# Performance work log

Hardware: AMD Instinct MI355X
Metric: run time of the kernel (lower is better)

The kernel has to match this reference:

```python
import jax, jax.numpy as jnp
import numpy as np

# --- config-derived constants (match init_kwargs) ---
BATCH = 16
TEMP = 0.1
N_REGIONS = 9
IMG = 512
NUM_FILTERS = 5      # len(no_filters)-1
N_DEC_BLOCKS = 2
SIZE_FACTOR = 1 << (NUM_FILTERS - N_DEC_BLOCKS)   # 8
IM = IMG // SIZE_FACTOR - 4                        # 60
H = W = IM + 2                                     # 62 (feature map spatial size)
C = 512
EPS = 1e-6

_h = IM // 2  # 30
_X = _Y = IM  # 60
POS = np.array([[0,0],[0,_h],[0,_Y],[_h,0],[_h,_h],[_h,_Y],[_X,0],[_X,_h],[_X,_Y]], np.int32)
NEG = np.array([
  [[0,_h],[_h,0],[_h,_h],[0,_Y],[_X,0]],
  [[0,0],[0,_Y],[_h,0],[_h,_h],[_h,_Y]],
  [[0,0],[0,_h],[_h,_h],[_h,_Y],[_X,_Y]],
  [[0,0],[0,_h],[_h,_h],[_X,0],[_X,_h]],
  [[0,0],[0,_h],[_h,0],[_h,_Y],[_X,_h]],
  [[0,_h],[0,_Y],[_h,_h],[_X,_h],[_X,_Y]],
  [[0,0],[_h,0],[_h,_h],[_X,_h],[_X,_Y]],
  [[_h,0],[_h,_h],[_h,_Y],[_X,0],[_X,_Y]],
  [[0,_Y],[_h,_h],[_h,_Y],[_X,0],[_X,_h]],
], np.int32)

def _patch_flat(idx):
    # idx [..., 2] (row, col) -> flat indices of the 2x2 patch, [..., 4]
    base = idx[..., 0] * W + idx[..., 1]
    return np.stack([base, base + 1, base + W, base + W + 1], axis=-1)

POS_FLAT = jnp.asarray(_patch_flat(POS))     # [9, 4]
NEG_FLAT = jnp.asarray(_patch_flat(NEG))     # [9, 5, 4]

def _cos(a, b):
    # cosine similarity over last axis, torch-style eps clamp on the norm product
    dot = jnp.sum(a * b, axis=-1)
    na = jnp.sqrt(jnp.sum(a * a, axis=-1))
    nb = jnp.sqrt(jnp.sum(b * b, axis=-1))
    return dot / jnp.maximum(na * nb, EPS)


def setup_inputs() -> dict:
    key = jax.random.key(0)
    x = jax.random.normal(key, (BATCH, C, H, W), dtype=jnp.float32)
    return {"x": x}


def reference(x):
    B = x.shape[0]
    xf = x.reshape(B, C, H * W)
    pp = xf[:, :, POS_FLAT]   # [B, C, 9, 4]
    nn_ = xf[:, :, NEG_FLAT]  # [B, C, 9, 5, 4]
    i1p, i2p = pp[0::2], pp[1::2]      # [P, C, 9, 4]
    i1n, i2n = nn_[0::2], nn_[1::2]    # [P, C, 9, 5, 4]

    # positive similarity (symmetric: cos(i1,i2) == cos(i2,i1))
    num_ss = _cos(i1p, i2p) / TEMP                 # [P, C, 9]
    S = jnp.sum(jnp.exp(num_ss), axis=1)           # [P, 9]

    a1 = i1p[:, :, :, None, :]                     # [P, C, 9, 1, 4]
    a2 = i2p[:, :, :, None, :]
    den1 = jnp.exp(_cos(a1, i1n) / TEMP) + jnp.exp(_cos(a1, i2n) / TEMP)  # [P, C, 9, 5]
    den2 = jnp.exp(_cos(a2, i2n) / TEMP) + jnp.exp(_cos(a2, i1n) / TEMP)
    D1 = jnp.sum(den1, axis=(1, 3))                # [P, 9]
    D2 = jnp.sum(den2, axis=(1, 3))

    loss = jnp.sum(-jnp.log(S / (S + D1)) - jnp.log(S / (S + D2)))
    return loss / B / N_REGIONS
```

## Files before the change

kernel.cpp:

```cpp
#include <hip/hip_runtime.h>
#include <math.h>

#define NPAIR 8
#define NREG 9
#define NCH 512
#define HW 3844
#define W62 62

__constant__ int POS_BASE[9] = {0, 30, 60, 1860, 1890, 1920, 3720, 3750, 3780};
__constant__ int NEG_BASE[9][5] = {
    {30, 1860, 1890, 60, 3720},
    {0, 60, 1860, 1890, 1920},
    {0, 30, 1890, 1920, 3780},
    {0, 30, 1890, 3720, 3750},
    {0, 30, 1860, 1920, 3750},
    {30, 60, 1890, 3750, 3780},
    {0, 1860, 1890, 3750, 3780},
    {1860, 1890, 1920, 3720, 3780},
    {60, 1890, 1920, 3720, 3750}};

__device__ __forceinline__ void load_patch(const float* __restrict__ p, int base, float v[4]) {
    float2 a = *(const float2*)(p + base);
    float2 b = *(const float2*)(p + base + W62);
    v[0] = a.x; v[1] = a.y; v[2] = b.x; v[3] = b.y;
}

__device__ __forceinline__ float dot4(const float* a, const float* b) {
    return a[0] * b[0] + a[1] * b[1] + a[2] * b[2] + a[3] * b[3];
}

__device__ __forceinline__ float wave_sum(float v) {
    #pragma unroll
    for (int off = 32; off > 0; off >>= 1) v += __shfl_down(v, off, 64);
    return v;
}

__global__ __launch_bounds__(512) void lcl_partial(const float* __restrict__ x,
                                                   float* __restrict__ ws) {
    const int blk = blockIdx.x;
    const int p = blk / NREG;
    const int r = blk % NREG;
    const int c = threadIdx.x;

    const float* p1 = x + ((size_t)(2 * p) * NCH + c) * HW;
    const float* p2 = x + ((size_t)(2 * p + 1) * NCH + c) * HW;

    float v1[4], v2[4], n1[5][4], n2[5][4];
    const int pb = POS_BASE[r];
    load_patch(p1, pb, v1);
    load_patch(p2, pb, v2);
    #pragma unroll
    for (int j = 0; j < 5; j++) {
        const int nb = NEG_BASE[r][j];
        load_patch(p1, nb, n1[j]);
        load_patch(p2, nb, n2[j]);
    }

    const float nv1 = dot4(v1, v1);
    const float nv2 = dot4(v2, v2);

    float s = expf(10.0f * dot4(v1, v2) / fmaxf(sqrtf(nv1 * nv2), 1e-6f));
    float d1 = 0.0f, d2 = 0.0f;
    #pragma unroll
    for (int j = 0; j < 5; j++) {
        const float nn1 = dot4(n1[j], n1[j]);
        const float nn2 = dot4(n2[j], n2[j]);
        d1 += expf(10.0f * dot4(v1, n1[j]) / fmaxf(sqrtf(nv1 * nn1), 1e-6f));
        d1 += expf(10.0f * dot4(v1, n2[j]) / fmaxf(sqrtf(nv1 * nn2), 1e-6f));
        d2 += expf(10.0f * dot4(v2, n2[j]) / fmaxf(sqrtf(nv2 * nn2), 1e-6f));
        d2 += expf(10.0f * dot4(v2, n1[j]) / fmaxf(sqrtf(nv2 * nn1), 1e-6f));
    }

    s = wave_sum(s);
    d1 = wave_sum(d1);
    d2 = wave_sum(d2);

    __shared__ float sm[3][8];
    const int wave = threadIdx.x >> 6;
    const int lane = threadIdx.x & 63;
    if (lane == 0) { sm[0][wave] = s; sm[1][wave] = d1; sm[2][wave] = d2; }
    __syncthreads();
    if (threadIdx.x == 0) {
        float S = 0.0f, D1 = 0.0f, D2 = 0.0f;
        #pragma unroll
        for (int w = 0; w < 8; w++) { S += sm[0][w]; D1 += sm[1][w]; D2 += sm[2][w]; }
        ws[blk] = logf(S + D1) + logf(S + D2) - 2.0f * logf(S);
    }
}

__global__ __launch_bounds__(64) void lcl_final(const float* __restrict__ ws,
                                                float* __restrict__ out) {
    const int t = threadIdx.x;
    float v = ws[t];
    if (t + 64 < NPAIR * NREG) v += ws[t + 64];
    v = wave_sum(v);
    if (t == 0) out[0] = v * (1.0f / 144.0f);
}

extern "C" void kernel_launch(void* const* d_in, const int* in_sizes, int n_in,
                              void* d_out, int out_size, void* d_ws, size_t ws_size,
                              hipStream_t stream) {
    const float* x = (const float*)d_in[0];
    float* out = (float*)d_out;
    float* ws = (float*)d_ws;

    lcl_partial<<<NPAIR * NREG, 512, 0, stream>>>(x, ws);
    lcl_final<<<1, 64, 0, stream>>>(ws, out);
}
```

Baseline: 172.0 us.

## Pre-gather unique 2x2 patches into a compact channel-major buffer

Measured after the change: 161.7 us. -6.0%, faster.

```diff
diff --git a/kernel.cpp b/kernel.cpp
--- a/kernel.cpp
+++ b/kernel.cpp
@@ -6,24 +6,21 @@
 #define NCH 512
 #define HW 3844
 #define W62 62
+#define NPATCH 9
 
-__constant__ int POS_BASE[9] = {0, 30, 60, 1860, 1890, 1920, 3720, 3750, 3780};
-__constant__ int NEG_BASE[9][5] = {
-    {30, 1860, 1890, 60, 3720},
-    {0, 60, 1860, 1890, 1920},
-    {0, 30, 1890, 1920, 3780},
-    {0, 30, 1890, 3720, 3750},
-    {0, 30, 1860, 1920, 3750},
-    {30, 60, 1890, 3750, 3780},
-    {0, 1860, 1890, 3750, 3780},
-    {1860, 1890, 1920, 3720, 3780},
-    {60, 1890, 1920, 3720, 3750}};
+__constant__ int PATCH_BASE[9] = {0, 30, 60, 1860, 1890, 1920, 3720, 3750, 3780};
+__constant__ int NEG_IDX[9][5] = {
+    {1, 3, 4, 2, 6},
+    {0, 2, 3, 4, 5},
+    {0, 1, 4, 5, 8},
+    {0, 1, 4, 6, 7},
+    {0, 1, 3, 5, 7},
+    {1, 2, 4, 7, 8},
+    {0, 3, 4, 7, 8},
+    {3, 4, 5, 6, 8},
+    {2, 4, 5, 6, 7}};
 
-__device__ __forceinline__ void load_patch(const float* __restrict__ p, int base, float v[4]) {
-    float2 a = *(const float2*)(p + base);
-    float2 b = *(const float2*)(p + base + W62);
-    v[0] = a.x; v[1] = a.y; v[2] = b.x; v[3] = b.y;
-}
+#define G_FLOATS (16 * NPATCH * 4 * NCH)
 
 __device__ __forceinline__ float dot4(const float* a, const float* b) {
     return a[0] * b[0] + a[1] * b[1] + a[2] * b[2] + a[3] * b[3];
@@ -35,25 +32,47 @@
     return v;
 }
 
-__global__ __launch_bounds__(512) void lcl_partial(const float* __restrict__ x,
-                                                   float* __restrict__ ws) {
+__global__ __launch_bounds__(256) void lcl_gather(const float* __restrict__ x,
+                                                  float* __restrict__ g) {
+    const int tid = blockIdx.x * 256 + threadIdx.x;
+    const int c = tid & (NCH - 1);
+    const int bp = tid >> 9;
+    const int patch = bp % NPATCH;
+    const int b = bp / NPATCH;
+    const float* src = x + (size_t)(b * NCH + c) * HW + PATCH_BASE[patch];
+    const float2 a0 = *(const float2*)(src);
+    const float2 a1 = *(const float2*)(src + W62);
+    float* dst = g + (size_t)bp * 4 * NCH + c;
+    dst[0] = a0.x;
+    dst[NCH] = a0.y;
+    dst[2 * NCH] = a1.x;
+    dst[3 * NCH] = a1.y;
+}
+
+__global__ __launch_bounds__(512) void lcl_partial(const float* __restrict__ g,
+                                                   float* __restrict__ terms) {
     const int blk = blockIdx.x;
     const int p = blk / NREG;
     const int r = blk % NREG;
     const int c = threadIdx.x;
 
-    const float* p1 = x + ((size_t)(2 * p) * NCH + c) * HW;
-    const float* p2 = x + ((size_t)(2 * p + 1) * NCH + c) * HW;
+    const float* g1 = g + (size_t)(2 * p) * NPATCH * 4 * NCH + c;
+    const float* g2 = g + (size_t)(2 * p + 1) * NPATCH * 4 * NCH + c;
 
     float v1[4], v2[4], n1[5][4], n2[5][4];
-    const int pb = POS_BASE[r];
-    load_patch(p1, pb, v1);
-    load_patch(p2, pb, v2);
+    #pragma unroll
+    for (int k = 0; k < 4; k++) {
+        v1[k] = g1[(r * 4 + k) * NCH];
+        v2[k] = g2[(r * 4 + k) * NCH];
+    }
     #pragma unroll
     for (int j = 0; j < 5; j++) {
-        const int nb = NEG_BASE[r][j];
-        load_patch(p1, nb, n1[j]);
-        load_patch(p2, nb, n2[j]);
+        const int q = NEG_IDX[r][j];
+        #pragma unroll
+        for (int k = 0; k < 4; k++) {
+            n1[j][k] = g1[(q * 4 + k) * NCH];
+            n2[j][k] = g2[(q * 4 + k) * NCH];
+        }
     }
 
     const float nv1 = dot4(v1, v1);
@@ -84,15 +103,15 @@
         float S = 0.0f, D1 = 0.0f, D2 = 0.0f;
         #pragma unroll
         for (int w = 0; w < 8; w++) { S += sm[0][w]; D1 += sm[1][w]; D2 += sm[2][w]; }
-        ws[blk] = logf(S + D1) + logf(S + D2) - 2.0f * logf(S);
+        terms[blk] = logf(S + D1) + logf(S + D2) - 2.0f * logf(S);
     }
 }
 
-__global__ __launch_bounds__(64) void lcl_final(const float* __restrict__ ws,
+__global__ __launch_bounds__(64) void lcl_final(const float* __restrict__ terms,
                                                 float* __restrict__ out) {
     const int t = threadIdx.x;
-    float v = ws[t];
-    if (t + 64 < NPAIR * NREG) v += ws[t + 64];
+    float v = terms[t];
+    if (t + 64 < NPAIR * NREG) v += terms[t + 64];
     v = wave_sum(v);
     if (t == 0) out[0] = v * (1.0f / 144.0f);
 }
@@ -102,8 +121,10 @@
                               hipStream_t stream) {
     const float* x = (const float*)d_in[0];
     float* out = (float*)d_out;
-    float* ws = (float*)d_ws;
+    float* g = (float*)d_ws;
+    float* terms = (float*)d_ws + G_FLOATS;
 
-    lcl_partial<<<NPAIR * NREG, 512, 0, stream>>>(x, ws);
-    lcl_final<<<1, 64, 0, stream>>>(ws, out);
+    lcl_gather<<<(16 * NPATCH * NCH) / 256, 256, 0, stream>>>(x, g);
+    lcl_partial<<<NPAIR * NREG, 512, 0, stream>>>(g, terms);
+    lcl_final<<<1, 64, 0, stream>>>(terms, out);
 }
```
